# Kernel tuning notes

Measured on AMD Instinct MI355X. Metric: run time of the kernel, lower is better.

The kernel has to match this reference:

```python
import jax, jax.numpy as jnp
import numpy as np

H = 256

def setup_inputs() -> dict:
    key = jax.random.key(0)
    ks = jax.random.split(key, 8)
    B, S = 32, 4096
    hidden = jax.random.normal(ks[0], (B, H), dtype=jnp.float32)
    encoder_outputs = jax.random.normal(ks[1], (B, S, H), dtype=jnp.float32)
    scale = 1.0 / np.sqrt(H)
    W1_w = jax.random.uniform(ks[2], (H, H), jnp.float32, -scale, scale)
    W1_b = jax.random.uniform(ks[3], (H,), jnp.float32, -scale, scale)
    W2_w = jax.random.uniform(ks[4], (H, H), jnp.float32, -scale, scale)
    W2_b = jax.random.uniform(ks[5], (H,), jnp.float32, -scale, scale)
    V_w = jax.random.uniform(ks[6], (H, 1), jnp.float32, -scale, scale)
    V_b = jax.random.uniform(ks[7], (1,), jnp.float32, -scale, scale)
    return {"hidden": hidden, "encoder_outputs": encoder_outputs,
            "W1_w": W1_w, "W1_b": W1_b, "W2_w": W2_w, "W2_b": W2_b,
            "V_w": V_w, "V_b": V_b}

def reference(hidden, encoder_outputs, W1_w, W1_b, W2_w, W2_b, V_w, V_b):
    # hidden: (B,H), encoder_outputs: (B,S,H)
    q = hidden @ W1_w + W1_b                     # (B,H)
    k = jnp.einsum('bsh,hd->bsd', encoder_outputs, W2_w) + W2_b  # (B,S,H)
    energy = jnp.tanh(q[:, None, :] + k)         # (B,S,H)
    scores = jnp.einsum('bsh,ho->bso', energy, V_w) + V_b        # (B,S,1)
    attention_weights = jax.nn.softmax(scores, axis=1)           # (B,S,1)
    context_vector = jnp.einsum('bso,bsh->bh', attention_weights, encoder_outputs)  # (B,H)
    return attention_weights, context_vector
```

## Files before the change

kernel.cpp:

```cpp
#include <hip/hip_runtime.h>
#include <hip/hip_bf16.h>
#include <math.h>

#define BB 32
#define SS 4096
#define HH 256

typedef __bf16 bf16x8 __attribute__((ext_vector_type(8)));
typedef float f32x4 __attribute__((ext_vector_type(4)));

#define GLOBAL_AS __attribute__((address_space(1)))
#define LDS_AS    __attribute__((address_space(3)))

__device__ inline bf16x8 cvt8(const float4& x, const float4& y) {
    union { __hip_bfloat162 p[4]; bf16x8 v; } u;
    u.p[0] = __float22bfloat162_rn(make_float2(x.x, x.y));
    u.p[1] = __float22bfloat162_rn(make_float2(x.z, x.w));
    u.p[2] = __float22bfloat162_rn(make_float2(y.x, y.y));
    u.p[3] = __float22bfloat162_rn(make_float2(y.z, y.w));
    return u.v;
}

__device__ inline float fast_tanh(float x) {
    float xc = fminf(fmaxf(x, -10.f), 10.f);
    float e  = __expf(2.f * xc);
    return (e - 1.f) * __builtin_amdgcn_rcpf(e + 1.f);
}

__global__ void prep_kernel(const float* __restrict__ W2_w,
                            ushort* __restrict__ w2sw,
                            const float* __restrict__ hidden,
                            const float* __restrict__ W1_w,
                            const float* __restrict__ W1_b,
                            const float* __restrict__ W2_b,
                            float* __restrict__ qq) {
    __shared__ float hid[HH];
    const int t = threadIdx.x;
    if (blockIdx.x < 256) {
        const int i = blockIdx.x * 256 + t;
        const int j    = i & 7;
        const int lane = (i >> 3) & 63;
        const int nt   = (i >> 9) & 15;
        const int kc   = i >> 13;
        const int k = kc * 32 + ((lane >> 4) & 3) * 8 + j;
        const int n = nt * 16 + (lane & 15);
        __hip_bfloat16 h = __float2bfloat16(W2_w[k * HH + n]);
        w2sw[i] = *(ushort*)&h;
    } else {
        const int b = blockIdx.x - 256;
        hid[t] = hidden[b * HH + t];
        __syncthreads();
        float acc = 0.f;
#pragma unroll 16
        for (int k = 0; k < HH; ++k)
            acc = fmaf(hid[k], W1_w[k * HH + t], acc);
        qq[b * HH + t] = acc + W1_b[t] + W2_b[t];
    }
}

__global__ __launch_bounds__(256, 4)
void score64_kernel(const float* __restrict__ enc,
                    const ushort* __restrict__ w2sw,
                    const float* __restrict__ qq,
                    const float* __restrict__ V_w,
                    const float* __restrict__ V_b,
                    float* __restrict__ scores,
                    float* __restrict__ mlpart) {
    __shared__ ushort w2buf[2][8192];
    __shared__ float sc_lds[64];

    const int t    = threadIdx.x;
    const int b    = blockIdx.y;
    const int s0   = blockIdx.x * 64;
    const int wave = t >> 6;
    const int lane = t & 63;
    const int l15  = lane & 15;
    const int quad = lane >> 4;

    f32x4 acc[16];
#pragma unroll
    for (int nt = 0; nt < 16; ++nt) acc[nt] = (f32x4)0.f;

    {
        const char* gsrc = (const char*)w2sw + t * 16;
        char* ldst = (char*)&w2buf[0][0] + wave * 1024;
#pragma unroll
        for (int i = 0; i < 4; ++i)
            __builtin_amdgcn_global_load_lds(
                (const GLOBAL_AS void*)(gsrc + i * 4096),
                (LDS_AS void*)(ldst + i * 4096), 16, 0, 0);
    }

    const float* aptr =
        enc + ((size_t)(b * SS + s0 + wave * 16 + l15)) * HH + quad * 8;
    float4 ax = *(const float4*)aptr;
    float4 ay = *(const float4*)(aptr + 4);

    for (int kc = 0; kc < 8; ++kc) {
        const int cur = kc & 1;
        __syncthreads();
        if (kc < 7) {
            const char* gsrc = (const char*)w2sw + (kc + 1) * 16384 + t * 16;
            char* ldst = (char*)&w2buf[cur ^ 1][0] + wave * 1024;
#pragma unroll
            for (int i = 0; i < 4; ++i)
                __builtin_amdgcn_global_load_lds(
                    (const GLOBAL_AS void*)(gsrc + i * 4096),
                    (LDS_AS void*)(ldst + i * 4096), 16, 0, 0);
        }
        bf16x8 af = cvt8(ax, ay);
        if (kc < 7) {
            ax = *(const float4*)(aptr + (kc + 1) * 32);
            ay = *(const float4*)(aptr + (kc + 1) * 32 + 4);
        }
#pragma unroll
        for (int nt = 0; nt < 16; ++nt) {
            bf16x8 bf = *(const bf16x8*)&w2buf[cur][(nt * 64 + lane) * 8];
            acc[nt] = __builtin_amdgcn_mfma_f32_16x16x32_bf16(af, bf, acc[nt], 0, 0, 0);
        }
    }

    float p[4] = {0.f, 0.f, 0.f, 0.f};
#pragma unroll
    for (int nt = 0; nt < 16; ++nt) {
        const int n = nt * 16 + l15;
        const float qn = qq[b * HH + n];
        const float vn = V_w[n];
#pragma unroll
        for (int r = 0; r < 4; ++r)
            p[r] = fmaf(vn, fast_tanh(qn + acc[nt][r]), p[r]);
    }
#pragma unroll
    for (int off = 1; off < 16; off <<= 1)
#pragma unroll
        for (int r = 0; r < 4; ++r)
            p[r] += __shfl_xor(p[r], off);

    const float vb = V_b[0];
    if (l15 == 0) {
        float4 pv = make_float4(p[0] + vb, p[1] + vb, p[2] + vb, p[3] + vb);
        const int row = wave * 16 + quad * 4;
        *(float4*)&sc_lds[row] = pv;
        *(float4*)&scores[b * SS + s0 + row] = pv;
    }
    __syncthreads();

    if (t < 64) {
        const float v = sc_lds[t];
        float m = v;
#pragma unroll
        for (int off = 1; off < 64; off <<= 1)
            m = fmaxf(m, __shfl_xor(m, off));
        float e = __expf(v - m);
#pragma unroll
        for (int off = 1; off < 64; off <<= 1)
            e += __shfl_xor(e, off);
        if (t == 0) {
            mlpart[(b * 64 + blockIdx.x) * 2]     = m;
            mlpart[(b * 64 + blockIdx.x) * 2 + 1] = e;
        }
    }
}

__global__ __launch_bounds__(256)
void ctx_kernel(const float* __restrict__ scores,
                const float* __restrict__ mlpart,
                const float* __restrict__ enc,
                float* __restrict__ weights_out,
                float* __restrict__ part) {
    __shared__ float wlds[128];
    __shared__ float accl[4][HH];
    __shared__ float mg_s, linv_s;

    const int t  = threadIdx.x;
    const int b  = blockIdx.y;
    const int c  = blockIdx.x;
    const int s0 = c * 128;

    if (t < 64) {
        const float2 ml = ((const float2*)mlpart)[b * 64 + t];
        float m = ml.x;
#pragma unroll
        for (int off = 1; off < 64; off <<= 1)
            m = fmaxf(m, __shfl_xor(m, off));
        float l = ml.y * __expf(ml.x - m);
#pragma unroll
        for (int off = 1; off < 64; off <<= 1)
            l += __shfl_xor(l, off);
        if (t == 0) { mg_s = m; linv_s = 1.f / l; }
    }
    __syncthreads();
    const float mg = mg_s, linv = linv_s;

    if (t < 128) {
        const float w = __expf(scores[b * SS + s0 + t] - mg) * linv;
        weights_out[b * SS + s0 + t] = w;
        wlds[t] = w;
    }
    __syncthreads();

    const int tr = t >> 6;
    const int h0 = (t & 63) * 4;
    float4 a = make_float4(0.f, 0.f, 0.f, 0.f);
    const float* ep = enc + ((size_t)(b * SS + s0)) * HH;
#pragma unroll 8
    for (int jj = 0; jj < 32; ++jj) {
        const int j = jj * 4 + tr;
        const float4 e = *(const float4*)(ep + (size_t)j * HH + h0);
        const float w = wlds[j];
        a.x = fmaf(w, e.x, a.x);
        a.y = fmaf(w, e.y, a.y);
        a.z = fmaf(w, e.z, a.z);
        a.w = fmaf(w, e.w, a.w);
    }
    *(float4*)&accl[tr][h0] = a;
    __syncthreads();

    const float s = accl[0][t] + accl[1][t] + accl[2][t] + accl[3][t];
    part[((size_t)(b * 32 + c)) * HH + t] = s;
}

__global__ void reduce_kernel(const float* __restrict__ part,
                              float* __restrict__ ctx_out) {
    const int b = blockIdx.x;
    const int h = threadIdx.x;
    float a = 0.f;
#pragma unroll 8
    for (int c = 0; c < 32; ++c) a += part[((size_t)(b * 32 + c)) * HH + h];
    ctx_out[b * HH + h] = a;
}

extern "C" void kernel_launch(void* const* d_in, const int* in_sizes, int n_in,
                              void* d_out, int out_size, void* d_ws, size_t ws_size,
                              hipStream_t stream) {
    const float* hidden = (const float*)d_in[0];
    const float* enc    = (const float*)d_in[1];
    const float* W1_w   = (const float*)d_in[2];
    const float* W1_b   = (const float*)d_in[3];
    const float* W2_w   = (const float*)d_in[4];
    const float* W2_b   = (const float*)d_in[5];
    const float* V_w    = (const float*)d_in[6];
    const float* V_b    = (const float*)d_in[7];

    float* out_weights = (float*)d_out;
    float* out_ctx     = (float*)d_out + BB * SS;

    float* ws      = (float*)d_ws;
    float* ws_qq   = ws;
    float* ws_sc   = ws_qq + BB * HH;
    float* ws_ml   = ws_sc + BB * SS;
    float* ws_part = ws_ml + BB * 64 * 2;
    ushort* ws_w2  = (ushort*)(ws_part + BB * 32 * HH);

    prep_kernel<<<dim3(256 + BB), dim3(256), 0, stream>>>(
        W2_w, ws_w2, hidden, W1_w, W1_b, W2_b, ws_qq);
    score64_kernel<<<dim3(SS / 64, BB), dim3(256), 0, stream>>>(
        enc, ws_w2, ws_qq, V_w, V_b, ws_sc, ws_ml);
    ctx_kernel<<<dim3(32, BB), dim3(256), 0, stream>>>(
        ws_sc, ws_ml, enc, out_weights, ws_part);
    reduce_kernel<<<dim3(BB), dim3(HH), 0, stream>>>(ws_part, out_ctx);
}
```

Baseline: 254.9 us.

## Use 2x2 wave tiling in score kernel and atomics for context reduction

The score kernel now splits its four waves into a 2x2 grid over rows and output columns. Each wave computes two 16-row M tiles against half of the N tiles, so every LDS B fragment feeds two MFMAs, which halves B reads from LDS per MFMA. The two halves of the partial scores are combined through LDS, which adds an extra sync. The context kernel uses 64-row chunks and atomically adds its partials into the zero-initialised output, which removes the separate reduce kernel and the partial buffer at the cost of a memset launch and atomic contention.

```diff
diff --git a/kernel.cpp b/kernel.cpp
--- a/kernel.cpp
+++ b/kernel.cpp
@@ -59,13 +59,13 @@
 }
 
 __global__ __launch_bounds__(256, 4)
-void score64_kernel(const float* __restrict__ enc,
-                    const ushort* __restrict__ w2sw,
-                    const float* __restrict__ qq,
-                    const float* __restrict__ V_w,
-                    const float* __restrict__ V_b,
-                    float* __restrict__ scores,
-                    float* __restrict__ mlpart) {
+void score_kernel(const float* __restrict__ enc,
+                  const ushort* __restrict__ w2sw,
+                  const float* __restrict__ qq,
+                  const float* __restrict__ V_w,
+                  const float* __restrict__ V_b,
+                  float* __restrict__ scores,
+                  float* __restrict__ mlpart) {
     __shared__ ushort w2buf[2][8192];
     __shared__ float sc_lds[64];
 
@@ -74,12 +74,16 @@
     const int s0   = blockIdx.x * 64;
     const int wave = t >> 6;
     const int lane = t & 63;
+    const int mw   = wave & 1;
+    const int nw   = wave >> 1;
     const int l15  = lane & 15;
     const int quad = lane >> 4;
 
-    f32x4 acc[16];
-#pragma unroll
-    for (int nt = 0; nt < 16; ++nt) acc[nt] = (f32x4)0.f;
+    f32x4 acc[2][8];
+#pragma unroll
+    for (int mt = 0; mt < 2; ++mt)
+#pragma unroll
+        for (int nt = 0; nt < 8; ++nt) acc[mt][nt] = (f32x4)0.f;
 
     {
         const char* gsrc = (const char*)w2sw + t * 16;
@@ -91,10 +95,11 @@
                 (LDS_AS void*)(ldst + i * 4096), 16, 0, 0);
     }
 
-    const float* aptr =
-        enc + ((size_t)(b * SS + s0 + wave * 16 + l15)) * HH + quad * 8;
-    float4 ax = *(const float4*)aptr;
-    float4 ay = *(const float4*)(aptr + 4);
+    const float* aptr0 =
+        enc + ((size_t)(b * SS + s0 + mw * 32 + l15)) * HH + quad * 8;
+    const float* aptr1 = aptr0 + (size_t)16 * HH;
+    float4 ax0 = *(const float4*)aptr0, ay0 = *(const float4*)(aptr0 + 4);
+    float4 ax1 = *(const float4*)aptr1, ay1 = *(const float4*)(aptr1 + 4);
 
     for (int kc = 0; kc < 8; ++kc) {
         const int cur = kc & 1;
@@ -108,40 +113,62 @@
                     (const GLOBAL_AS void*)(gsrc + i * 4096),
                     (LDS_AS void*)(ldst + i * 4096), 16, 0, 0);
         }
-        bf16x8 af = cvt8(ax, ay);
+        bf16x8 af0 = cvt8(ax0, ay0);
+        bf16x8 af1 = cvt8(ax1, ay1);
         if (kc < 7) {
-            ax = *(const float4*)(aptr + (kc + 1) * 32);
-            ay = *(const float4*)(aptr + (kc + 1) * 32 + 4);
-        }
-#pragma unroll
-        for (int nt = 0; nt < 16; ++nt) {
-            bf16x8 bf = *(const bf16x8*)&w2buf[cur][(nt * 64 + lane) * 8];
-            acc[nt] = __builtin_amdgcn_mfma_f32_16x16x32_bf16(af, bf, acc[nt], 0, 0, 0);
-        }
-    }
-
-    float p[4] = {0.f, 0.f, 0.f, 0.f};
-#pragma unroll
-    for (int nt = 0; nt < 16; ++nt) {
-        const int n = nt * 16 + l15;
+            const int o = (kc + 1) * 32;
+            ax0 = *(const float4*)(aptr0 + o);
+            ay0 = *(const float4*)(aptr0 + o + 4);
+            ax1 = *(const float4*)(aptr1 + o);
+            ay1 = *(const float4*)(aptr1 + o + 4);
+        }
+#pragma unroll
+        for (int nt = 0; nt < 8; ++nt) {
+            bf16x8 bf =
+                *(const bf16x8*)&w2buf[cur][((nw * 8 + nt) * 64 + lane) * 8];
+            acc[0][nt] = __builtin_amdgcn_mfma_f32_16x16x32_bf16(af0, bf, acc[0][nt], 0, 0, 0);
+            acc[1][nt] = __builtin_amdgcn_mfma_f32_16x16x32_bf16(af1, bf, acc[1][nt], 0, 0, 0);
+        }
+    }
+
+    float p[2][4] = {{0.f, 0.f, 0.f, 0.f}, {0.f, 0.f, 0.f, 0.f}};
+#pragma unroll
+    for (int nt = 0; nt < 8; ++nt) {
+        const int n = nw * 128 + nt * 16 + l15;
         const float qn = qq[b * HH + n];
         const float vn = V_w[n];
 #pragma unroll
-        for (int r = 0; r < 4; ++r)
-            p[r] = fmaf(vn, fast_tanh(qn + acc[nt][r]), p[r]);
+        for (int mt = 0; mt < 2; ++mt)
+#pragma unroll
+            for (int r = 0; r < 4; ++r)
+                p[mt][r] = fmaf(vn, fast_tanh(qn + acc[mt][nt][r]), p[mt][r]);
     }
 #pragma unroll
     for (int off = 1; off < 16; off <<= 1)
 #pragma unroll
-        for (int r = 0; r < 4; ++r)
-            p[r] += __shfl_xor(p[r], off);
-
+        for (int mt = 0; mt < 2; ++mt)
+#pragma unroll
+            for (int r = 0; r < 4; ++r)
+                p[mt][r] += __shfl_xor(p[mt][r], off);
+
+    if (nw == 0 && l15 == 0) {
+#pragma unroll
+        for (int mt = 0; mt < 2; ++mt)
+            *(float4*)&sc_lds[mw * 32 + mt * 16 + quad * 4] =
+                make_float4(p[mt][0], p[mt][1], p[mt][2], p[mt][3]);
+    }
+    __syncthreads();
     const float vb = V_b[0];
-    if (l15 == 0) {
-        float4 pv = make_float4(p[0] + vb, p[1] + vb, p[2] + vb, p[3] + vb);
-        const int row = wave * 16 + quad * 4;
-        *(float4*)&sc_lds[row] = pv;
-        *(float4*)&scores[b * SS + s0 + row] = pv;
+    if (nw == 1 && l15 == 0) {
+#pragma unroll
+        for (int mt = 0; mt < 2; ++mt) {
+            const int row = mw * 32 + mt * 16 + quad * 4;
+            float4 h = *(const float4*)&sc_lds[row];
+            float4 v = make_float4(h.x + p[mt][0] + vb, h.y + p[mt][1] + vb,
+                                   h.z + p[mt][2] + vb, h.w + p[mt][3] + vb);
+            *(float4*)&sc_lds[row] = v;
+            *(float4*)&scores[b * SS + s0 + row] = v;
+        }
     }
     __syncthreads();
 
@@ -167,15 +194,15 @@
                 const float* __restrict__ mlpart,
                 const float* __restrict__ enc,
                 float* __restrict__ weights_out,
-                float* __restrict__ part) {
-    __shared__ float wlds[128];
+                float* __restrict__ ctx_out) {
+    __shared__ float wlds[64];
     __shared__ float accl[4][HH];
     __shared__ float mg_s, linv_s;
 
     const int t  = threadIdx.x;
     const int b  = blockIdx.y;
     const int c  = blockIdx.x;
-    const int s0 = c * 128;
+    const int s0 = c * 64;
 
     if (t < 64) {
         const float2 ml = ((const float2*)mlpart)[b * 64 + t];
@@ -192,7 +219,7 @@
     __syncthreads();
     const float mg = mg_s, linv = linv_s;
 
-    if (t < 128) {
+    if (t < 64) {
         const float w = __expf(scores[b * SS + s0 + t] - mg) * linv;
         weights_out[b * SS + s0 + t] = w;
         wlds[t] = w;
@@ -203,8 +230,8 @@
     const int h0 = (t & 63) * 4;
     float4 a = make_float4(0.f, 0.f, 0.f, 0.f);
     const float* ep = enc + ((size_t)(b * SS + s0)) * HH;
-#pragma unroll 8
-    for (int jj = 0; jj < 32; ++jj) {
+#pragma unroll
+    for (int jj = 0; jj < 16; ++jj) {
         const int j = jj * 4 + tr;
         const float4 e = *(const float4*)(ep + (size_t)j * HH + h0);
         const float w = wlds[j];
@@ -217,17 +244,7 @@
     __syncthreads();
 
     const float s = accl[0][t] + accl[1][t] + accl[2][t] + accl[3][t];
-    part[((size_t)(b * 32 + c)) * HH + t] = s;
-}
-
-__global__ void reduce_kernel(const float* __restrict__ part,
-                              float* __restrict__ ctx_out) {
-    const int b = blockIdx.x;
-    const int h = threadIdx.x;
-    float a = 0.f;
-#pragma unroll 8
-    for (int c = 0; c < 32; ++c) a += part[((size_t)(b * 32 + c)) * HH + h];
-    ctx_out[b * HH + h] = a;
+    atomicAdd(&ctx_out[b * HH + t], s);
 }
 
 extern "C" void kernel_launch(void* const* d_in, const int* in_sizes, int n_in,
@@ -245,18 +262,17 @@
     float* out_weights = (float*)d_out;
     float* out_ctx     = (float*)d_out + BB * SS;
 
-    float* ws      = (float*)d_ws;
-    float* ws_qq   = ws;
-    float* ws_sc   = ws_qq + BB * HH;
-    float* ws_ml   = ws_sc + BB * SS;
-    float* ws_part = ws_ml + BB * 64 * 2;
-    ushort* ws_w2  = (ushort*)(ws_part + BB * 32 * HH);
-
+    float* ws     = (float*)d_ws;
+    float* ws_qq  = ws;
+    float* ws_sc  = ws_qq + BB * HH;
+    float* ws_ml  = ws_sc + BB * SS;
+    ushort* ws_w2 = (ushort*)(ws_ml + BB * 64 * 2);
+
+    hipMemsetAsync(out_ctx, 0, BB * HH * sizeof(float), stream);
     prep_kernel<<<dim3(256 + BB), dim3(256), 0, stream>>>(
         W2_w, ws_w2, hidden, W1_w, W1_b, W2_b, ws_qq);
-    score64_kernel<<<dim3(SS / 64, BB), dim3(256), 0, stream>>>(
+    score_kernel<<<dim3(SS / 64, BB), dim3(256), 0, stream>>>(
         enc, ws_w2, ws_qq, V_w, V_b, ws_sc, ws_ml);
-    ctx_kernel<<<dim3(32, BB), dim3(256), 0, stream>>>(
-        ws_sc, ws_ml, enc, out_weights, ws_part);
-    reduce_kernel<<<dim3(BB), dim3(HH), 0, stream>>>(ws_part, out_ctx);
-}
+    ctx_kernel<<<dim3(64, BB), dim3(256), 0, stream>>>(
+        ws_sc, ws_ml, enc, out_weights, out_ctx);
+}
```

New measurement: 255.2 us. No clear change (+0.1%).
